# Kernel optimization log

Hardware: AMD Instinct MI355X
Metric: run time of the kernel (lower is better)

Reference implementation:

```python
import jax, jax.numpy as jnp
import numpy as np

EMBED_DIM = 1024
HEAD_DIM = 64
B, S = 8, 2048


def setup_inputs() -> dict:
    key = jax.random.key(0)
    ks = jax.random.split(key, 8)
    s_in = 1.0 / np.sqrt(EMBED_DIM)
    return {
        "x": jax.random.normal(ks[0], (B, S, EMBED_DIM), dtype=jnp.float32),
        "y": jax.random.normal(ks[1], (B, S, EMBED_DIM), dtype=jnp.float32),
        "Wq": jax.random.normal(ks[2], (EMBED_DIM, HEAD_DIM), dtype=jnp.float32) * s_in,
        "bq": jnp.zeros((HEAD_DIM,), dtype=jnp.float32),
        "Wk": jax.random.normal(ks[3], (EMBED_DIM, HEAD_DIM), dtype=jnp.float32) * s_in,
        "bk": jnp.zeros((HEAD_DIM,), dtype=jnp.float32),
        "Wv": jax.random.normal(ks[4], (EMBED_DIM, HEAD_DIM), dtype=jnp.float32) * s_in,
        "bv": jnp.zeros((HEAD_DIM,), dtype=jnp.float32),
    }


def reference(x, y, Wq, bq, Wk, bk, Wv, bv):
    # single-head attention; mask=True -> tril applied PRE-softmax (zeros, not -inf)
    q = jnp.einsum("bse,eh->bsh", y, Wq) + bq  # [B,S,H]
    k = jnp.einsum("bse,eh->bsh", x, Wk) + bk
    v = jnp.einsum("bse,eh->bsh", x, Wv) + bv
    scale = 1.0 / jnp.sqrt(jnp.float32(HEAD_DIM))
    scores = jnp.einsum("bqh,bkh->bqk", q, k) * scale  # [B,S,S]
    scores = jnp.tril(scores)  # faithful: zero upper triangle BEFORE softmax
    attn = jax.nn.softmax(scores, axis=-1)
    return jnp.einsum("bqk,bkh->bqh", attn, v)  # [B,S,H]
```

## Files before the change

### kernel.cpp

```cpp
#include <hip/hip_runtime.h>

#define SEQ 2048
#define EMB 1024
#define HD 64

typedef _Float16 f16x8 __attribute__((ext_vector_type(8)));
typedef _Float16 f16x4 __attribute__((ext_vector_type(4)));
typedef float f32x4 __attribute__((ext_vector_type(4)));

__device__ __forceinline__ f32x4 mfma32(f16x8 a, f16x8 b, f32x4 c) {
    return __builtin_amdgcn_mfma_f32_16x16x32_f16(a, b, c, 0, 0, 0);
}
__device__ __forceinline__ f32x4 mfma16(f16x4 a, f16x4 b, f32x4 c) {
    return __builtin_amdgcn_mfma_f32_16x16x16f16(a, b, c, 0, 0, 0);
}

__global__ __launch_bounds__(256) void wcvt_kernel(
    const float* __restrict__ Wq, const float* __restrict__ Wk,
    const float* __restrict__ Wv, _Float16* __restrict__ Wf)
{
    const int m = blockIdx.x >> 2, nt = blockIdx.x & 3;
    const float* __restrict__ W = (m == 0) ? Wq : (m == 1) ? Wk : Wv;
    const int tid = threadIdx.x;
    #pragma unroll
    for (int i = 0; i < 8; ++i) {
        int linear = i * 256 + tid;
        int kc = linear >> 6, ln = linear & 63;
        int q8 = (ln >> 4) * 8, l = ln & 15;
        f16x8 w;
        #pragma unroll
        for (int j = 0; j < 8; ++j)
            w[j] = (_Float16)W[(size_t)(kc * 32 + q8 + j) * 64 + nt * 16 + l];
        *(f16x8*)&Wf[((size_t)((m * 4 + nt) * 32 + kc)) * 512 + (size_t)ln * 8] = w;
    }
}

__global__ __launch_bounds__(256) void proj_kernel(
    const float* __restrict__ x, const float* __restrict__ y,
    const _Float16* __restrict__ Wf,
    const float* __restrict__ bq, const float* __restrict__ bk,
    const float* __restrict__ bv,
    _Float16* __restrict__ Qb, _Float16* __restrict__ Kf,
    _Float16* __restrict__ Vf, float* __restrict__ Vts)
{
    const int mode = blockIdx.y;
    const int r0 = blockIdx.x * 64;
    const int tid = threadIdx.x;
    const int wave = tid >> 6, lane = tid & 63;
    const int l15 = lane & 15, quad = lane >> 4;

    __shared__ float TL[64][65];

    const float* __restrict__ src = mode ? x : y;
    const _Float16* __restrict__ WA = Wf + (mode ? 65536 : 0);
    const _Float16* __restrict__ WB = Wf + 131072;

    f32x4 zero = {0.f, 0.f, 0.f, 0.f};
    f32x4 acc0[4], acc1[4];
    #pragma unroll
    for (int i = 0; i < 4; ++i) { acc0[i] = zero; acc1[i] = zero; }

    const float* arow = src + (size_t)(r0 + wave * 16 + l15) * 1024 + quad * 8;
    const int lo8 = lane * 8;

    #pragma unroll 4
    for (int kc = 0; kc < 32; ++kc) {
        float4 a0 = *(const float4*)(arow + kc * 32);
        float4 a1 = *(const float4*)(arow + kc * 32 + 4);
        f16x8 af;
        af[0] = (_Float16)a0.x; af[1] = (_Float16)a0.y;
        af[2] = (_Float16)a0.z; af[3] = (_Float16)a0.w;
        af[4] = (_Float16)a1.x; af[5] = (_Float16)a1.y;
        af[6] = (_Float16)a1.z; af[7] = (_Float16)a1.w;
        #pragma unroll
        for (int nt = 0; nt < 4; ++nt) {
            f16x8 b0 = *(const f16x8*)&WA[((size_t)(nt * 32 + kc)) * 512 + lo8];
            acc0[nt] = mfma32(af, b0, acc0[nt]);
        }
        if (mode) {
            #pragma unroll
            for (int nt = 0; nt < 4; ++nt) {
                f16x8 b1 = *(const f16x8*)&WB[((size_t)(nt * 32 + kc)) * 512 + lo8];
                acc1[nt] = mfma32(af, b1, acc1[nt]);
            }
        }
    }

    if (mode == 0) {
        #pragma unroll
        for (int nt = 0; nt < 4; ++nt) {
            int h = nt * 16 + l15;
            float bs = bq[h];
            #pragma unroll
            for (int r = 0; r < 4; ++r) {
                int row = r0 + wave * 16 + quad * 4 + r;
                Qb[(size_t)row * 64 + h] = (_Float16)(acc0[nt][r] + bs);
            }
        }
    } else {
        const int bb = r0 >> 11, s0 = r0 & (SEQ - 1);
        #pragma unroll
        for (int nt = 0; nt < 4; ++nt) {
            int h = nt * 16 + l15;
            float bs = bk[h];
            #pragma unroll
            for (int r = 0; r < 4; ++r)
                TL[wave * 16 + quad * 4 + r][h] = acc0[nt][r] + bs;
        }
        __syncthreads();
        {
            int c = tid >> 6, ln = tid & 63, q8 = (ln >> 4) * 8, l = ln & 15;
            #pragma unroll
            for (int half = 0; half < 2; ++half) {
                f16x8 w;
                #pragma unroll
                for (int j = 0; j < 8; ++j)
                    w[j] = (_Float16)TL[c * 16 + l][half * 32 + q8 + j];
                *(f16x8*)&Kf[(((size_t)(bb * 128 + (s0 >> 4) + c)) * 2 + half) * 512 + ln * 8] = w;
            }
        }
        __syncthreads();
        #pragma unroll
        for (int nt = 0; nt < 4; ++nt) {
            int h = nt * 16 + l15;
            float bs = bv[h];
            #pragma unroll
            for (int r = 0; r < 4; ++r)
                TL[wave * 16 + quad * 4 + r][h] = acc1[nt][r] + bs;
        }
        __syncthreads();
        {
            int ht = tid >> 6, ln = tid & 63, q4 = (ln >> 4) * 4, l = ln & 15;
            #pragma unroll
            for (int c2 = 0; c2 < 2; ++c2) {
                f16x8 w;
                #pragma unroll
                for (int j = 0; j < 8; ++j)
                    w[j] = (_Float16)TL[c2 * 32 + ((j >> 2) << 4) + q4 + (j & 3)][ht * 16 + l];
                *(f16x8*)&Vf[(((size_t)(bb * 64 + (s0 >> 5) + c2)) * 4 + ht) * 512 + ln * 8] = w;
            }
            int h = tid & 63, wv = tid >> 6;
            float s = 0.f;
            #pragma unroll
            for (int i = 0; i < 16; ++i) s += TL[wv * 16 + i][h];
            Vts[((size_t)bb * 128 + (s0 >> 4) + wv) * 64 + h] = s;
        }
    }
}

__global__ __launch_bounds__(256) void vsuf_kernel(
    const float* __restrict__ Vts, float* __restrict__ Vsuf)
{
    const int b = blockIdx.x, hh = blockIdx.y;
    const int tid = threadIdx.x;
    const int seg = tid >> 5, hl = tid & 31, h = (hh << 5) + hl;
    __shared__ float segsum[8][33];
    float vals[16];
    const float* src = Vts + ((size_t)b * 128 + seg * 16) * 64 + h;
    float s = 0.f;
    #pragma unroll
    for (int i = 0; i < 16; ++i) { vals[i] = src[i * 64]; s += vals[i]; }
    segsum[seg][hl] = s;
    __syncthreads();
    float run = 0.f;
    #pragma unroll
    for (int ss = 7; ss >= 0; --ss) if (ss > seg) run += segsum[ss][hl];
    float* dst = Vsuf + ((size_t)b * 128 + seg * 16) * 64 + h;
    #pragma unroll
    for (int i = 15; i >= 0; --i) { run += vals[i]; dst[i * 64] = run; }
}

__global__ __launch_bounds__(256) void attn_kernel(
    const _Float16* __restrict__ Qb, const _Float16* __restrict__ Kf,
    const _Float16* __restrict__ Vf, const float* __restrict__ Vsuf,
    float* __restrict__ out)
{
    const int b = blockIdx.y;
    const int tpair = blockIdx.x;
    const int tid = threadIdx.x;
    const int wave = tid >> 6, lane = tid & 63;
    const int l15 = lane & 15, quad = lane >> 4;

    __shared__ float part[4][16][68];
    __shared__ float lpart[4][16];

    const f16x4 ONES4 = {(_Float16)1.f, (_Float16)1.f, (_Float16)1.f, (_Float16)1.f};
    f32x4 zero = {0.f, 0.f, 0.f, 0.f};

    const _Float16* __restrict__ kfb = Kf + (size_t)b * 131072 + lane * 8;
    const _Float16* __restrict__ vfb = Vf + (size_t)b * 131072 + lane * 8;

    #pragma unroll 1
    for (int sel = 0; sel < 2; ++sel) {
        const int tq = sel ? (127 - tpair) : tpair;
        const int qbase = tq << 4;
        const int nk2 = (tq >> 1) + 1;

        const _Float16* qp = Qb + ((size_t)(b * SEQ + qbase + l15) << 6);
        f16x8 qf0 = *(const f16x8*)(qp + quad * 8);
        f16x8 qf1 = *(const f16x8*)(qp + 32 + quad * 8);

        f32x4 accO[4];
        #pragma unroll
        for (int i = 0; i < 4; ++i) accO[i] = zero;
        f32x4 accL = zero;
        const int qg = qbase + l15;

        f16x8 R0[8], R1[8];
        int kc2 = wave;
        {
            int i0 = (kc2 < nk2) ? kc2 : 0;
            const _Float16* kp = kfb + (size_t)i0 * 2048;
            const _Float16* vp = vfb + (size_t)i0 * 2048;
            R0[0] = *(const f16x8*)(kp);        R0[1] = *(const f16x8*)(kp + 512);
            R0[2] = *(const f16x8*)(kp + 1024); R0[3] = *(const f16x8*)(kp + 1536);
            R0[4] = *(const f16x8*)(vp);        R0[5] = *(const f16x8*)(vp + 512);
            R0[6] = *(const f16x8*)(vp + 1024); R0[7] = *(const f16x8*)(vp + 1536);
        }

        for (; kc2 < nk2; kc2 += 4) {
            int nx = kc2 + 4;
            int nxi = (nx < nk2) ? nx : kc2;
            {
                const _Float16* kp = kfb + (size_t)nxi * 2048;
                const _Float16* vp = vfb + (size_t)nxi * 2048;
                R1[0] = *(const f16x8*)(kp);        R1[1] = *(const f16x8*)(kp + 512);
                R1[2] = *(const f16x8*)(kp + 1024); R1[3] = *(const f16x8*)(kp + 1536);
                R1[4] = *(const f16x8*)(vp);        R1[5] = *(const f16x8*)(vp + 512);
                R1[6] = *(const f16x8*)(vp + 1024); R1[7] = *(const f16x8*)(vp + 1536);
            }
            #pragma unroll
            for (int c = 0; c < 2; ++c) {
                const int kc = 2 * kc2 + c;
                f32x4 s = zero;
                s = mfma32(R0[2 * c], qf0, s);
                s = mfma32(R0[2 * c + 1], qf1, s);
                const float oneval = (kc <= tq) ? 1.0f : 0.0f;
                const int kqb = (kc << 4) + (quad << 2);
                f16x4 pf;
                #pragma unroll
                for (int r = 0; r < 4; ++r) {
                    float w = (kqb + r <= qg) ? __expf(s[r] * 0.125f) : oneval;
                    pf[r] = (_Float16)w;
                }
                #pragma unroll
                for (int ht = 0; ht < 4; ++ht) {
                    f16x8 vv = R0[4 + ht];
                    f16x4 vh;
                    if (c == 0) { vh[0] = vv[0]; vh[1] = vv[1]; vh[2] = vv[2]; vh[3] = vv[3]; }
                    else        { vh[0] = vv[4]; vh[1] = vv[5]; vh[2] = vv[6]; vh[3] = vv[7]; }
                    accO[ht] = mfma16(vh, pf, accO[ht]);
                }
                accL = mfma16(ONES4, pf, accL);
            }
            #pragma unroll
            for (int i = 0; i < 8; ++i) R0[i] = R1[i];
        }

        #pragma unroll
        for (int ht = 0; ht < 4; ++ht)
            #pragma unroll
            for (int r = 0; r < 4; ++r)
                part[wave][l15][ht * 16 + quad * 4 + r] = accO[ht][r];
        if (quad == 0) lpart[wave][l15] = accL[0];
        __syncthreads();

        {
            const int q = tid >> 4, hb = (tid & 15) << 2;
            f32x4 o = zero;
            float l = 0.f;
            #pragma unroll
            for (int w = 0; w < 4; ++w) {
                f32x4 pw = *(const f32x4*)&part[w][q][hb];
                o = o + pw;
                l += lpart[w][q];
            }
            const int tend = tq + 1;
            const float nOnes = (float)(SEQ - (tend << 4));
            f32x4 cs = zero;
            if (tend < 128)
                cs = *(const f32x4*)&Vsuf[((size_t)(b * 128 + tend) << 6) + hb];
            const float inv = 1.0f / (l + nOnes);
            f32x4 res = (o + cs) * inv;
            *(f32x4*)&out[((size_t)(b * SEQ + qbase + q) << 6) + hb] = res;
        }
        __syncthreads();
    }
}

extern "C" void kernel_launch(void* const* d_in, const int* in_sizes, int n_in,
                              void* d_out, int out_size, void* d_ws, size_t ws_size,
                              hipStream_t stream) {
    const float* x  = (const float*)d_in[0];
    const float* y  = (const float*)d_in[1];
    const float* Wq = (const float*)d_in[2];
    const float* bq = (const float*)d_in[3];
    const float* Wk = (const float*)d_in[4];
    const float* bk = (const float*)d_in[5];
    const float* Wv = (const float*)d_in[6];
    const float* bv = (const float*)d_in[7];
    float* out = (float*)d_out;

    char* ws = (char*)d_ws;
    _Float16* Qb  = (_Float16*)(ws);
    _Float16* Kf  = (_Float16*)(ws + (1u << 21));
    _Float16* Vf  = (_Float16*)(ws + (2u << 21));
    _Float16* Wf  = (_Float16*)(ws + (3u << 21));
    float*    Vts = (float*)(ws + (3u << 21) + (512u << 10));
    float*    Vsf = (float*)(ws + (3u << 21) + (768u << 10));

    wcvt_kernel<<<dim3(12), 256, 0, stream>>>(Wq, Wk, Wv, Wf);
    proj_kernel<<<dim3(256, 2), 256, 0, stream>>>(x, y, Wf, bq, bk, bv, Qb, Kf, Vf, Vts);
    vsuf_kernel<<<dim3(8, 2), 256, 0, stream>>>(Vts, Vsf);
    attn_kernel<<<dim3(64, 8), 256, 0, stream>>>(Qb, Kf, Vf, Vsf, out);
}
```

Baseline: 210.0 us.

## Split-K projection with 512 threads and 32-row query tiles in attention

The projection kernel now runs 8 waves per block, splitting the 1024-wide reduction into two halves combined through shared memory. It also adds explicit register prefetching of A and B fragments several steps ahead. The attention kernel drops the paired 16-row tiles and gives each block one 32-row query tile, so each loaded K/V fragment feeds two query sub-tiles, with double-buffered K/V loads. This aims to raise memory-level parallelism in the bandwidth-bound projection and halve K/V traffic in attention, at the cost of more registers, an extra LDS reduction, and possibly less even load balance across blocks.

Result: faster. 197.2 us (-6.1%).

```diff
diff --git a/kernel.cpp b/kernel.cpp
--- a/kernel.cpp
+++ b/kernel.cpp
@@ -35,7 +35,7 @@
     }
 }
 
-__global__ __launch_bounds__(256) void proj_kernel(
+__global__ __launch_bounds__(512) void proj_kernel(
     const float* __restrict__ x, const float* __restrict__ y,
     const _Float16* __restrict__ Wf,
     const float* __restrict__ bq, const float* __restrict__ bk,
@@ -48,6 +48,7 @@
     const int tid = threadIdx.x;
     const int wave = tid >> 6, lane = tid & 63;
     const int l15 = lane & 15, quad = lane >> 4;
+    const int rowgrp = wave >> 1, khalf = wave & 1;
 
     __shared__ float TL[64][65];
 
@@ -60,85 +61,120 @@
     #pragma unroll
     for (int i = 0; i < 4; ++i) { acc0[i] = zero; acc1[i] = zero; }
 
-    const float* arow = src + (size_t)(r0 + wave * 16 + l15) * 1024 + quad * 8;
+    const float* arow = src + (size_t)(r0 + rowgrp * 16 + l15) * 1024 + khalf * 512 + quad * 8;
     const int lo8 = lane * 8;
-
-    #pragma unroll 4
-    for (int kc = 0; kc < 32; ++kc) {
-        float4 a0 = *(const float4*)(arow + kc * 32);
-        float4 a1 = *(const float4*)(arow + kc * 32 + 4);
+    const int kb = khalf * 16;
+
+    float4 A0[4], A1[4];
+    f16x8 Bq[2][4], Bv[2][4];
+
+    auto LDA = [&](int d, int kc) {
+        const float4* p = (const float4*)(arow + kc * 32);
+        A0[d] = p[0]; A1[d] = p[1];
+    };
+    auto LDB = [&](int d, int kc) {
+        #pragma unroll
+        for (int nt = 0; nt < 4; ++nt)
+            Bq[d][nt] = *(const f16x8*)&WA[((size_t)(nt * 32 + kb + kc)) * 512 + lo8];
+        if (mode) {
+            #pragma unroll
+            for (int nt = 0; nt < 4; ++nt)
+                Bv[d][nt] = *(const f16x8*)&WB[((size_t)(nt * 32 + kb + kc)) * 512 + lo8];
+        }
+    };
+
+    LDA(0, 0); LDA(1, 1); LDA(2, 2); LDA(3, 3);
+    LDB(0, 0); LDB(1, 1);
+
+    #pragma unroll
+    for (int kc = 0; kc < 16; ++kc) {
+        const int sa = kc & 3, sb = kc & 1;
         f16x8 af;
-        af[0] = (_Float16)a0.x; af[1] = (_Float16)a0.y;
-        af[2] = (_Float16)a0.z; af[3] = (_Float16)a0.w;
-        af[4] = (_Float16)a1.x; af[5] = (_Float16)a1.y;
-        af[6] = (_Float16)a1.z; af[7] = (_Float16)a1.w;
+        af[0] = (_Float16)A0[sa].x; af[1] = (_Float16)A0[sa].y;
+        af[2] = (_Float16)A0[sa].z; af[3] = (_Float16)A0[sa].w;
+        af[4] = (_Float16)A1[sa].x; af[5] = (_Float16)A1[sa].y;
+        af[6] = (_Float16)A1[sa].z; af[7] = (_Float16)A1[sa].w;
+        #pragma unroll
+        for (int nt = 0; nt < 4; ++nt)
+            acc0[nt] = mfma32(af, Bq[sb][nt], acc0[nt]);
+        if (mode) {
+            #pragma unroll
+            for (int nt = 0; nt < 4; ++nt)
+                acc1[nt] = mfma32(af, Bv[sb][nt], acc1[nt]);
+        }
+        if (kc < 12) LDA(sa, kc + 4);
+        if (kc < 14) LDB(sb, kc + 2);
+    }
+
+    const float* __restrict__ bias0 = mode ? bk : bq;
+    const int bb = r0 >> 11, s0 = r0 & (SEQ - 1);
+
+    if (khalf == 1) {
+        #pragma unroll
+        for (int nt = 0; nt < 4; ++nt)
+            #pragma unroll
+            for (int r = 0; r < 4; ++r)
+                TL[rowgrp * 16 + quad * 4 + r][nt * 16 + l15] = acc0[nt][r];
+    }
+    __syncthreads();
+    if (khalf == 0) {
         #pragma unroll
         for (int nt = 0; nt < 4; ++nt) {
-            f16x8 b0 = *(const f16x8*)&WA[((size_t)(nt * 32 + kc)) * 512 + lo8];
-            acc0[nt] = mfma32(af, b0, acc0[nt]);
-        }
-        if (mode) {
+            float bs = bias0[nt * 16 + l15];
+            #pragma unroll
+            for (int r = 0; r < 4; ++r) {
+                int rr = rowgrp * 16 + quad * 4 + r;
+                TL[rr][nt * 16 + l15] = acc0[nt][r] + TL[rr][nt * 16 + l15] + bs;
+            }
+        }
+    }
+    __syncthreads();
+
+    if (mode == 0) {
+        int row = tid >> 3, c8 = (tid & 7) * 8;
+        f16x8 o;
+        #pragma unroll
+        for (int j = 0; j < 8; ++j) o[j] = (_Float16)TL[row][c8 + j];
+        *(f16x8*)&Qb[(size_t)(r0 + row) * 64 + c8] = o;
+    } else {
+        {
+            int c = tid >> 7, hf = (tid >> 6) & 1, ln = tid & 63;
+            f16x8 w;
+            #pragma unroll
+            for (int j = 0; j < 8; ++j)
+                w[j] = (_Float16)TL[c * 16 + (ln & 15)][hf * 32 + ((ln >> 4) << 3) + j];
+            *(f16x8*)&Kf[(((size_t)(bb * 128 + (s0 >> 4) + c)) * 2 + hf) * 512 + ln * 8] = w;
+        }
+        __syncthreads();
+        if (khalf == 1) {
+            #pragma unroll
+            for (int nt = 0; nt < 4; ++nt)
+                #pragma unroll
+                for (int r = 0; r < 4; ++r)
+                    TL[rowgrp * 16 + quad * 4 + r][nt * 16 + l15] = acc1[nt][r];
+        }
+        __syncthreads();
+        if (khalf == 0) {
             #pragma unroll
             for (int nt = 0; nt < 4; ++nt) {
-                f16x8 b1 = *(const f16x8*)&WB[((size_t)(nt * 32 + kc)) * 512 + lo8];
-                acc1[nt] = mfma32(af, b1, acc1[nt]);
+                float bs = bv[nt * 16 + l15];
+                #pragma unroll
+                for (int r = 0; r < 4; ++r) {
+                    int rr = rowgrp * 16 + quad * 4 + r;
+                    TL[rr][nt * 16 + l15] = acc1[nt][r] + TL[rr][nt * 16 + l15] + bs;
+                }
             }
-        }
-    }
-
-    if (mode == 0) {
-        #pragma unroll
-        for (int nt = 0; nt < 4; ++nt) {
-            int h = nt * 16 + l15;
-            float bs = bq[h];
-            #pragma unroll
-            for (int r = 0; r < 4; ++r) {
-                int row = r0 + wave * 16 + quad * 4 + r;
-                Qb[(size_t)row * 64 + h] = (_Float16)(acc0[nt][r] + bs);
-            }
-        }
-    } else {
-        const int bb = r0 >> 11, s0 = r0 & (SEQ - 1);
-        #pragma unroll
-        for (int nt = 0; nt < 4; ++nt) {
-            int h = nt * 16 + l15;
-            float bs = bk[h];
-            #pragma unroll
-            for (int r = 0; r < 4; ++r)
-                TL[wave * 16 + quad * 4 + r][h] = acc0[nt][r] + bs;
         }
         __syncthreads();
         {
-            int c = tid >> 6, ln = tid & 63, q8 = (ln >> 4) * 8, l = ln & 15;
-            #pragma unroll
-            for (int half = 0; half < 2; ++half) {
-                f16x8 w;
-                #pragma unroll
-                for (int j = 0; j < 8; ++j)
-                    w[j] = (_Float16)TL[c * 16 + l][half * 32 + q8 + j];
-                *(f16x8*)&Kf[(((size_t)(bb * 128 + (s0 >> 4) + c)) * 2 + half) * 512 + ln * 8] = w;
-            }
-        }
-        __syncthreads();
-        #pragma unroll
-        for (int nt = 0; nt < 4; ++nt) {
-            int h = nt * 16 + l15;
-            float bs = bv[h];
-            #pragma unroll
-            for (int r = 0; r < 4; ++r)
-                TL[wave * 16 + quad * 4 + r][h] = acc1[nt][r] + bs;
-        }
-        __syncthreads();
-        {
-            int ht = tid >> 6, ln = tid & 63, q4 = (ln >> 4) * 4, l = ln & 15;
-            #pragma unroll
-            for (int c2 = 0; c2 < 2; ++c2) {
-                f16x8 w;
-                #pragma unroll
-                for (int j = 0; j < 8; ++j)
-                    w[j] = (_Float16)TL[c2 * 32 + ((j >> 2) << 4) + q4 + (j & 3)][ht * 16 + l];
-                *(f16x8*)&Vf[(((size_t)(bb * 64 + (s0 >> 5) + c2)) * 4 + ht) * 512 + ln * 8] = w;
-            }
+            int c2 = tid >> 8, ht = (tid >> 6) & 3, ln = tid & 63;
+            f16x8 w;
+            #pragma unroll
+            for (int j = 0; j < 8; ++j)
+                w[j] = (_Float16)TL[c2 * 32 + ((j >> 2) << 4) + ((ln >> 4) << 2) + (j & 3)][ht * 16 + (ln & 15)];
+            *(f16x8*)&Vf[(((size_t)(bb * 64 + (s0 >> 5) + c2)) * 4 + ht) * 512 + ln * 8] = w;
+        }
+        if (tid < 256) {
             int h = tid & 63, wv = tid >> 6;
             float s = 0.f;
             #pragma unroll
@@ -176,115 +212,127 @@
     float* __restrict__ out)
 {
     const int b = blockIdx.y;
-    const int tpair = blockIdx.x;
+    const int tq = blockIdx.x;
     const int tid = threadIdx.x;
     const int wave = tid >> 6, lane = tid & 63;
     const int l15 = lane & 15, quad = lane >> 4;
 
-    __shared__ float part[4][16][68];
-    __shared__ float lpart[4][16];
+    __shared__ float part[4][32][68];
+    __shared__ float lpart[4][32];
 
     const f16x4 ONES4 = {(_Float16)1.f, (_Float16)1.f, (_Float16)1.f, (_Float16)1.f};
     f32x4 zero = {0.f, 0.f, 0.f, 0.f};
 
+    const int qbase = tq << 5;
+    const int qgA = qbase + l15, qgB = qgA + 16;
+
+    const _Float16* qpA = Qb + ((size_t)(b * SEQ + qbase + l15) << 6);
+    const _Float16* qpB = qpA + (16 << 6);
+    f16x8 qfA0 = *(const f16x8*)(qpA + quad * 8);
+    f16x8 qfA1 = *(const f16x8*)(qpA + 32 + quad * 8);
+    f16x8 qfB0 = *(const f16x8*)(qpB + quad * 8);
+    f16x8 qfB1 = *(const f16x8*)(qpB + 32 + quad * 8);
+
+    f32x4 accOA[4], accOB[4], accLA = zero, accLB = zero;
+    #pragma unroll
+    for (int i = 0; i < 4; ++i) { accOA[i] = zero; accOB[i] = zero; }
+
     const _Float16* __restrict__ kfb = Kf + (size_t)b * 131072 + lane * 8;
     const _Float16* __restrict__ vfb = Vf + (size_t)b * 131072 + lane * 8;
 
-    #pragma unroll 1
-    for (int sel = 0; sel < 2; ++sel) {
-        const int tq = sel ? (127 - tpair) : tpair;
-        const int qbase = tq << 4;
-        const int nk2 = (tq >> 1) + 1;
-
-        const _Float16* qp = Qb + ((size_t)(b * SEQ + qbase + l15) << 6);
-        f16x8 qf0 = *(const f16x8*)(qp + quad * 8);
-        f16x8 qf1 = *(const f16x8*)(qp + 32 + quad * 8);
-
-        f32x4 accO[4];
-        #pragma unroll
-        for (int i = 0; i < 4; ++i) accO[i] = zero;
-        f32x4 accL = zero;
-        const int qg = qbase + l15;
-
-        f16x8 R0[8], R1[8];
-        int kc2 = wave;
-        {
-            int i0 = (kc2 < nk2) ? kc2 : 0;
-            const _Float16* kp = kfb + (size_t)i0 * 2048;
-            const _Float16* vp = vfb + (size_t)i0 * 2048;
-            R0[0] = *(const f16x8*)(kp);        R0[1] = *(const f16x8*)(kp + 512);
-            R0[2] = *(const f16x8*)(kp + 1024); R0[3] = *(const f16x8*)(kp + 1536);
-            R0[4] = *(const f16x8*)(vp);        R0[5] = *(const f16x8*)(vp + 512);
-            R0[6] = *(const f16x8*)(vp + 1024); R0[7] = *(const f16x8*)(vp + 1536);
-        }
-
-        for (; kc2 < nk2; kc2 += 4) {
-            int nx = kc2 + 4;
-            int nxi = (nx < nk2) ? nx : kc2;
-            {
-                const _Float16* kp = kfb + (size_t)nxi * 2048;
-                const _Float16* vp = vfb + (size_t)nxi * 2048;
-                R1[0] = *(const f16x8*)(kp);        R1[1] = *(const f16x8*)(kp + 512);
-                R1[2] = *(const f16x8*)(kp + 1024); R1[3] = *(const f16x8*)(kp + 1536);
-                R1[4] = *(const f16x8*)(vp);        R1[5] = *(const f16x8*)(vp + 512);
-                R1[6] = *(const f16x8*)(vp + 1024); R1[7] = *(const f16x8*)(vp + 1536);
+    f16x8 k0[4], v0[4], k1[4], v1[4];
+
+    auto LDK = [&](f16x8* kd, f16x8* vd, int kc2) {
+        const _Float16* kp = kfb + (size_t)kc2 * 2048;
+        kd[0] = *(const f16x8*)(kp);
+        kd[1] = *(const f16x8*)(kp + 512);
+        kd[2] = *(const f16x8*)(kp + 1024);
+        kd[3] = *(const f16x8*)(kp + 1536);
+        const _Float16* vp = vfb + (size_t)kc2 * 2048;
+        vd[0] = *(const f16x8*)(vp);
+        vd[1] = *(const f16x8*)(vp + 512);
+        vd[2] = *(const f16x8*)(vp + 1024);
+        vd[3] = *(const f16x8*)(vp + 1536);
+    };
+
+    auto CMP = [&](const f16x8* kd, const f16x8* vd, int kc2) {
+        #pragma unroll
+        for (int c = 0; c < 2; ++c) {
+            f32x4 sA = zero, sB = zero;
+            sA = mfma32(kd[2 * c], qfA0, sA);
+            sA = mfma32(kd[2 * c + 1], qfA1, sA);
+            sB = mfma32(kd[2 * c], qfB0, sB);
+            sB = mfma32(kd[2 * c + 1], qfB1, sB);
+            const int kqb = (kc2 << 5) + (c << 4) + (quad << 2);
+            f16x4 pfA, pfB;
+            #pragma unroll
+            for (int r = 0; r < 4; ++r) {
+                pfA[r] = (_Float16)((kqb + r <= qgA) ? __expf(sA[r] * 0.125f) : 1.0f);
+                pfB[r] = (_Float16)((kqb + r <= qgB) ? __expf(sB[r] * 0.125f) : 1.0f);
             }
             #pragma unroll
-            for (int c = 0; c < 2; ++c) {
-                const int kc = 2 * kc2 + c;
-                f32x4 s = zero;
-                s = mfma32(R0[2 * c], qf0, s);
-                s = mfma32(R0[2 * c + 1], qf1, s);
-                const float oneval = (kc <= tq) ? 1.0f : 0.0f;
-                const int kqb = (kc << 4) + (quad << 2);
-                f16x4 pf;
-                #pragma unroll
-                for (int r = 0; r < 4; ++r) {
-                    float w = (kqb + r <= qg) ? __expf(s[r] * 0.125f) : oneval;
-                    pf[r] = (_Float16)w;
-                }
-                #pragma unroll
-                for (int ht = 0; ht < 4; ++ht) {
-                    f16x8 vv = R0[4 + ht];
-                    f16x4 vh;
-                    if (c == 0) { vh[0] = vv[0]; vh[1] = vv[1]; vh[2] = vv[2]; vh[3] = vv[3]; }
-                    else        { vh[0] = vv[4]; vh[1] = vv[5]; vh[2] = vv[6]; vh[3] = vv[7]; }
-                    accO[ht] = mfma16(vh, pf, accO[ht]);
-                }
-                accL = mfma16(ONES4, pf, accL);
+            for (int ht = 0; ht < 4; ++ht) {
+                f16x8 vv = vd[ht];
+                f16x4 vh;
+                if (c == 0) { vh[0] = vv[0]; vh[1] = vv[1]; vh[2] = vv[2]; vh[3] = vv[3]; }
+                else        { vh[0] = vv[4]; vh[1] = vv[5]; vh[2] = vv[6]; vh[3] = vv[7]; }
+                accOA[ht] = mfma16(vh, pfA, accOA[ht]);
+                accOB[ht] = mfma16(vh, pfB, accOB[ht]);
             }
-            #pragma unroll
-            for (int i = 0; i < 8; ++i) R0[i] = R1[i];
-        }
-
-        #pragma unroll
-        for (int ht = 0; ht < 4; ++ht)
-            #pragma unroll
-            for (int r = 0; r < 4; ++r)
-                part[wave][l15][ht * 16 + quad * 4 + r] = accO[ht][r];
-        if (quad == 0) lpart[wave][l15] = accL[0];
-        __syncthreads();
-
-        {
-            const int q = tid >> 4, hb = (tid & 15) << 2;
-            f32x4 o = zero;
-            float l = 0.f;
-            #pragma unroll
-            for (int w = 0; w < 4; ++w) {
-                f32x4 pw = *(const f32x4*)&part[w][q][hb];
-                o = o + pw;
-                l += lpart[w][q];
-            }
-            const int tend = tq + 1;
-            const float nOnes = (float)(SEQ - (tend << 4));
-            f32x4 cs = zero;
-            if (tend < 128)
-                cs = *(const f32x4*)&Vsuf[((size_t)(b * 128 + tend) << 6) + hb];
-            const float inv = 1.0f / (l + nOnes);
-            f32x4 res = (o + cs) * inv;
-            *(f32x4*)&out[((size_t)(b * SEQ + qbase + q) << 6) + hb] = res;
-        }
-        __syncthreads();
+            accLA = mfma16(ONES4, pfA, accLA);
+            accLB = mfma16(ONES4, pfB, accLB);
+        }
+    };
+
+    const int n2 = tq + 1;
+    int i = wave;
+    LDK(k0, v0, (i < n2) ? i : 0);
+    for (; i < n2; i += 8) {
+        const int i1 = i + 4;
+        LDK(k1, v1, (i1 < n2) ? i1 : i);
+        CMP(k0, v0, i);
+        const int i2 = i + 8;
+        LDK(k0, v0, (i2 < n2) ? i2 : i);
+        if (i1 < n2) CMP(k1, v1, i1);
+    }
+
+    #pragma unroll
+    for (int ht = 0; ht < 4; ++ht)
+        #pragma unroll
+        for (int r = 0; r < 4; ++r) {
+            part[wave][l15][ht * 16 + quad * 4 + r] = accOA[ht][r];
+            part[wave][16 + l15][ht * 16 + quad * 4 + r] = accOB[ht][r];
+        }
+    if (quad == 0) {
+        lpart[wave][l15] = accLA[0];
+        lpart[wave][16 + l15] = accLB[0];
+    }
+    __syncthreads();
+
+    {
+        const int q = tid >> 3, hb = (tid & 7) << 3;
+        f32x4 o0 = zero, o1 = zero;
+        float l = 0.f;
+        #pragma unroll
+        for (int w = 0; w < 4; ++w) {
+            l += lpart[w][q];
+            o0 = o0 + *(const f32x4*)&part[w][q][hb];
+            o1 = o1 + *(const f32x4*)&part[w][q][hb + 4];
+        }
+        const int tend = 2 * tq + 2;
+        const float nOnes = (float)(SEQ - (tend << 4));
+        f32x4 cs0 = zero, cs1 = zero;
+        if (tend < 128) {
+            const float* cp = &Vsuf[((size_t)(b * 128 + tend) << 6) + hb];
+            cs0 = *(const f32x4*)(cp);
+            cs1 = *(const f32x4*)(cp + 4);
+        }
+        const float inv = 1.0f / (l + nOnes);
+        f32x4 r0 = (o0 + cs0) * inv;
+        f32x4 r1 = (o1 + cs1) * inv;
+        float* op = &out[((size_t)(b * SEQ + qbase + q) << 6) + hb];
+        *(f32x4*)(op) = r0;
+        *(f32x4*)(op + 4) = r1;
     }
 }
 
@@ -310,7 +358,7 @@
     float*    Vsf = (float*)(ws + (3u << 21) + (768u << 10));
 
     wcvt_kernel<<<dim3(12), 256, 0, stream>>>(Wq, Wk, Wv, Wf);
-    proj_kernel<<<dim3(256, 2), 256, 0, stream>>>(x, y, Wf, bq, bk, bv, Qb, Kf, Vf, Vts);
+    proj_kernel<<<dim3(256, 2), 512, 0, stream>>>(x, y, Wf, bq, bk, bv, Qb, Kf, Vf, Vts);
     vsuf_kernel<<<dim3(8, 2), 256, 0, stream>>>(Vts, Vsf);
     attn_kernel<<<dim3(64, 8), 256, 0, stream>>>(Qb, Kf, Vf, Vsf, out);
 }
```
